# Kernel optimization log

Hardware: AMD Instinct MI355X
Metric: run time of the kernel (lower is better)

## Reference

```python
import jax, jax.numpy as jnp
import numpy as np

SIGMA = 25.0
EPS = 1e-5
TWO_PI = 2.0 * np.pi


def _gn(x, gamma, beta, groups):
    # GroupNorm over (C//G, H, W) per group, per-channel affine.
    B, C, H, W = x.shape
    xg = x.reshape(B, groups, -1)
    m = xg.mean(-1, keepdims=True)
    v = xg.var(-1, keepdims=True)
    xn = ((xg - m) * jax.lax.rsqrt(v + EPS)).reshape(B, C, H, W)
    return xn * gamma[None, :, None, None] + beta[None, :, None, None]


def _conv3(x, k, b):
    y = jax.lax.conv_general_dilated(x, k, (1, 1), 'SAME',
                                     dimension_numbers=('NCHW', 'OIHW', 'NCHW'))
    return y + b[None, :, None, None]


def _tconv2(x, k, b):
    # ConvTranspose2d kernel=2 stride=2 (no overlap) == einsum + reshape.
    # k: [C_in, C_out, 2, 2]
    B, C, H, W = x.shape
    O = k.shape[1]
    y = jnp.einsum('bchw,codq->bohdwq', x, k).reshape(B, O, 2 * H, 2 * W)
    return y + b[None, :, None, None]


def _conv1(x, k, b):
    # 1x1 conv; k: [C_out, C_in]
    return jnp.einsum('bchw,oc->bohw', x, k) + b[None, :, None, None]


def _pool(x):
    B, C, H, W = x.shape
    return x.reshape(B, C, H // 2, 2, W // 2, 2).max(axis=(3, 5))


def _std(t):
    return jnp.sqrt((SIGMA ** (2.0 * t) - 1.0) / (2.0 * jnp.log(SIGMA)))


def setup_inputs() -> dict:
    key = jax.random.key(0)
    ks = jax.random.split(key, 16)
    B, H, W = 64, 128, 128
    E = 2 * W  # 256 = embed_dim

    def w(k, shape, fan_in):
        return jax.random.normal(k, shape, jnp.float32) / np.sqrt(fan_in)

    inp = {
        'x': jax.random.normal(ks[0], (B, 1, H, W), jnp.float32),
        't': jax.random.uniform(ks[1], (B,), jnp.float32, 1e-3, 1.0),
        'Wf': jax.random.normal(ks[2], (H, W), jnp.float32) * 30.0,  # fixed Fourier features
        'fc1_w': w(ks[3], (E, E), E),
        'fc1_b': jnp.zeros((E,), jnp.float32),
        'conv1_k': w(ks[4], (6, 1, 3, 3), 9),
        'conv1_b': jnp.zeros((6,), jnp.float32),
        'gn1_g': jnp.ones((6,), jnp.float32), 'gn1_b': jnp.zeros((6,), jnp.float32),
        'conv2_k': w(ks[5], (24, 6, 3, 3), 6 * 9),
        'conv2_b': jnp.zeros((24,), jnp.float32),
        'gn2_g': jnp.ones((24,), jnp.float32), 'gn2_b': jnp.zeros((24,), jnp.float32),
        't3_k': w(ks[6], (24, 24, 2, 2), 24 * 4),
        't3_b': jnp.zeros((24,), jnp.float32),
        'gn3_g': jnp.ones((48,), jnp.float32), 'gn3_b': jnp.zeros((48,), jnp.float32),
        't4_k': w(ks[7], (48, 12, 2, 2), 48 * 4),
        't4_b': jnp.zeros((12,), jnp.float32),
        'gn4_g': jnp.ones((18,), jnp.float32), 'gn4_b': jnp.zeros((18,), jnp.float32),
        't5_k': w(ks[8], (6, 18), 18),
        't5_b': jnp.zeros((6,), jnp.float32),
        'gn5_g': jnp.ones((6,), jnp.float32), 'gn5_b': jnp.zeros((6,), jnp.float32),
        'fin_k': w(ks[9], (1, 6), 6),
        'fin_b': jnp.zeros((1,), jnp.float32),
    }
    return inp


def reference(x, t, Wf, fc1_w, fc1_b, conv1_k, conv1_b, gn1_g, gn1_b,
              conv2_k, conv2_b, gn2_g, gn2_b, t3_k, t3_b, gn3_g, gn3_b,
              t4_k, t4_b, gn4_g, gn4_b, t5_k, t5_b, gn5_g, gn5_b,
              fin_k, fin_b):
    # Vectorized Gaussian Fourier projection: [B,1,H,W] -> [B,1,H,2W]
    p = x * Wf[None, None] * TWO_PI
    xe = jnp.concatenate([jnp.sin(p), jnp.cos(p)], axis=-1)
    # fc1 on last dim (embed_dim = 2W)
    xf = jnp.einsum('bchw,ow->bcho', xe, fc1_w) + fc1_b
    c1 = _conv3(xf, conv1_k, conv1_b)                              # [B,6,H,2W]
    p1 = _pool(jax.nn.relu(_gn(c1, gn1_g, gn1_b, 6)))              # [B,6,H/2,W]
    c2 = _conv3(p1, conv2_k, conv2_b)                              # [B,24,H/2,W]
    p2 = _pool(jax.nn.relu(_gn(c2, gn2_g, gn2_b, 24)))             # [B,24,H/4,W/2]
    a = p2 * jax.nn.sigmoid(p2)                                    # SiLU bottleneck
    u3 = _tconv2(a, t3_k, t3_b)                                    # [B,24,H/2,W]
    g3 = _gn(jnp.concatenate([c2, u3], axis=1), gn3_g, gn3_b, 6)   # 48 ch
    u4 = _tconv2(g3, t4_k, t4_b)                                   # [B,12,H,2W]
    g4 = _gn(jnp.concatenate([c1, u4], axis=1), gn4_g, gn4_b, 6)   # 18 ch
    u5 = _conv1(g4, t5_k, t5_b)                                    # [B,6,H,2W]
    g5 = _gn(u5, gn5_g, gn5_b, 6)
    return _conv1(g5, fin_k, fin_b) / _std(t)[:, None, None, None]
```

## Files before the change

kernel.cpp:

```cpp
#include <hip/hip_runtime.h>
#include <hip/hip_bf16.h>
#include <math.h>

#define BB 64
#define HH 128
#define WW 128
#define EE 256
#define HP (HH*EE)
#define H2 64
#define W2 128
#define PL2 (H2*W2)
#define H4 32
#define W4 64
#define PL4 (H4*W4)

typedef __hip_bfloat16 bf;
typedef unsigned short ushortt;
typedef __attribute__((ext_vector_type(8))) __bf16 b8v;
typedef __attribute__((ext_vector_type(4))) float f4v;

__device__ __forceinline__ float tof(bf v)    { return __bfloat162float(v); }
__device__ __forceinline__ bf    tob(float v) { return __float2bfloat16(v); }
__device__ __forceinline__ unsigned int bfbits(float v) {
    return (unsigned int)__builtin_bit_cast(ushortt, __float2bfloat16(v));
}
__device__ __forceinline__ float b2f(unsigned int u16) {
    unsigned int x = u16 << 16;
    return __builtin_bit_cast(float, x);
}
__device__ __forceinline__ void wred2(float& s, float& q) {
    #pragma unroll
    for (int m = 32; m; m >>= 1) {
        s += __shfl_xor(s, m);
        q += __shfl_xor(q, m);
    }
}

__global__ __launch_bounds__(256) void k_fourier_fc1(
    const float* __restrict__ x, const float* __restrict__ Wf,
    const float* __restrict__ fc1_w, const float* __restrict__ fc1_b,
    bf* __restrict__ xf, float* __restrict__ mb)
{
    __shared__ ushortt sA[64*264];
    __shared__ ushortt sB[64*264];
    int t = threadIdx.x;
    for (int i = blockIdx.x*256 + t; i < 9216; i += 512*256) mb[i] = 0.f;
    int rb = blockIdx.x >> 2, cb = blockIdx.x & 3;
    int row0 = rb*64, col0 = cb*64;
    const float TP = 6.2831853071795864769f;
    for (int it = 0; it < 32; ++it) {
        int i = it*256 + t;
        int r = i >> 7, w = i & 127;
        int rg = row0 + r;
        float p = x[(size_t)rg*WW + w] * Wf[(size_t)(rg & (HH-1))*WW + w] * TP;
        sA[r*264 + w]       = (ushortt)bfbits(__sinf(p));
        sA[r*264 + 128 + w] = (ushortt)bfbits(__cosf(p));
    }
    #pragma unroll
    for (int it = 0; it < 16; ++it) {
        int i = it*256 + t;
        int o = i >> 6, c4 = i & 63;
        float4 w4 = *(const float4*)(fc1_w + (size_t)(col0 + o)*EE + c4*4);
        uint2 pk;
        pk.x = bfbits(w4.x) | (bfbits(w4.y) << 16);
        pk.y = bfbits(w4.z) | (bfbits(w4.w) << 16);
        *(uint2*)&sB[o*264 + c4*4] = pk;
    }
    __syncthreads();
    int lane = t & 63, wid = t >> 6;
    int m = lane & 15, kq = (lane >> 4) * 8;
    f4v acc[4] = {};
    const ushortt* aBase = &sA[(wid*16 + m)*264 + kq];
    #pragma unroll
    for (int k0 = 0; k0 < 8; ++k0) {
        b8v av = *(const b8v*)(aBase + k0*32);
        #pragma unroll
        for (int t4 = 0; t4 < 4; ++t4) {
            b8v bv = *(const b8v*)&sB[(t4*16 + m)*264 + k0*32 + kq];
            acc[t4] = __builtin_amdgcn_mfma_f32_16x16x32_bf16(av, bv, acc[t4], 0, 0, 0);
        }
    }
    int rbase = row0 + wid*16 + (lane >> 4)*4;
    #pragma unroll
    for (int t4 = 0; t4 < 4; ++t4) {
        int col = col0 + t4*16 + m;
        float bias = fc1_b[col];
        #pragma unroll
        for (int r = 0; r < 4; ++r)
            xf[(size_t)(rbase + r)*EE + col] = tob(acc[t4][r] + bias);
    }
}

__global__ __launch_bounds__(256) void k_conv1(
    const bf* __restrict__ xf, const float* __restrict__ k,
    const float* __restrict__ bias, bf* __restrict__ c1, float* __restrict__ mc1)
{
    __shared__ ushortt sT[6*272];
    __shared__ float red[4][6][2];
    int t = threadIdx.x;
    int ht = blockIdx.x & 31, b = blockIdx.x >> 5;
    int h0 = ht*4;
    const bf* src = xf + (size_t)b*HP;
    if (t < 192) {
        int r = t >> 5, i = t & 31;
        int gy = h0 - 1 + r;
        uint4 v = {0,0,0,0};
        if (gy >= 0 && gy < HH) v = *(const uint4*)(src + (size_t)gy*EE + i*8);
        *(uint4*)&sT[r*272 + 8 + i*8] = v;
    } else if (t < 204) {
        int e = t - 192;
        int r = e >> 1, s = e & 1;
        uint4 z = {0,0,0,0};
        *(uint4*)&sT[r*272 + s*264] = z;
    }
    __syncthreads();
    int wq = (t & 63)*4, hl = t >> 6;
    int lane = t & 63, wid = t >> 6;
    float v[3][6];
    #pragma unroll
    for (int ky = 0; ky < 3; ++ky)
      #pragma unroll
      for (int j = 0; j < 6; ++j)
        v[ky][j] = b2f((unsigned)sT[(hl+ky)*272 + 7 + wq + j]);
    int h = h0 + hl;
    #pragma unroll
    for (int o = 0; o < 6; ++o) {
        float bv = bias[o];
        float a0=bv, a1=bv, a2=bv, a3=bv;
        #pragma unroll
        for (int ky = 0; ky < 3; ++ky)
          #pragma unroll
          for (int kx = 0; kx < 3; ++kx) {
            float wv = k[o*9 + ky*3 + kx];
            a0 += v[ky][kx+0]*wv;
            a1 += v[ky][kx+1]*wv;
            a2 += v[ky][kx+2]*wv;
            a3 += v[ky][kx+3]*wv;
          }
        uint2 pk;
        pk.x = bfbits(a0) | (bfbits(a1) << 16);
        pk.y = bfbits(a2) | (bfbits(a3) << 16);
        *(uint2*)(c1 + ((size_t)(b*6+o)*HH + h)*EE + wq) = pk;
        float s = a0+a1+a2+a3, q = a0*a0+a1*a1+a2*a2+a3*a3;
        wred2(s, q);
        if (lane == 0) { red[wid][o][0] = s; red[wid][o][1] = q; }
    }
    __syncthreads();
    if (t < 6) {
        float S = 0.f, Q = 0.f;
        #pragma unroll
        for (int wv = 0; wv < 4; ++wv) { S += red[wv][t][0]; Q += red[wv][t][1]; }
        atomicAdd(&mc1[((size_t)b*6 + t)*2],     S);
        atomicAdd(&mc1[((size_t)b*6 + t)*2 + 1], Q);
    }
}

__global__ __launch_bounds__(256) void k_conv2(
    const bf* __restrict__ c1, const float* __restrict__ mc1,
    const float* __restrict__ g1, const float* __restrict__ be1,
    const float* __restrict__ kw, const float* __restrict__ bias,
    bf* __restrict__ c2, float* __restrict__ mc2)
{
    __shared__ ushortt sA[256*64];
    __shared__ ushortt sW[32*64];
    __shared__ ushortt sP[6*4*136];
    __shared__ float ssl[12];
    __shared__ float redS[24], redQ[24];
    int t = threadIdx.x;
    int ht = blockIdx.x & 31, b = blockIdx.x >> 5;
    int h0 = ht*2;
    int lane = t & 63, wid = t >> 6;
    int m = lane & 15, q4 = lane >> 4;
    if (t < 24) { redS[t] = 0.f; redQ[t] = 0.f; }
    if (t < 6) {
        float s = mc1[((size_t)b*6 + t)*2], q = mc1[((size_t)b*6 + t)*2 + 1];
        float mean = s * (1.f/HP);
        float var  = q * (1.f/HP) - mean*mean;
        float rstd = rsqrtf(var + 1e-5f);
        float sc = g1[t]*rstd;
        ssl[t*2] = sc; ssl[t*2+1] = be1[t] - mean*sc;
    }
    for (int i = t; i < 1024; i += 256) ((unsigned*)sW)[i] = 0;
    __syncthreads();
    for (int i = t; i < 3120; i += 256) {
        int c = i / 520, rem = i % 520;
        int ry = rem / 130, rx = rem % 130;
        int gy = h0 - 1 + ry, gx = rx - 1;
        float v = 0.f;
        if (gy >= 0 && gy < H2 && gx >= 0 && gx < W2) {
            const bf* pp = c1 + ((size_t)(b*6+c)*HH + 2*gy)*EE + 2*gx;
            unsigned r0 = *(const unsigned*)pp;
            unsigned r1 = *(const unsigned*)(pp + EE);
            float sc = ssl[c*2], sh = ssl[c*2+1];
            float e0 = fmaxf(b2f(r0 & 0xffff)*sc+sh, 0.f);
            float e1 = fmaxf(b2f(r0 >> 16)   *sc+sh, 0.f);
            float e2 = fmaxf(b2f(r1 & 0xffff)*sc+sh, 0.f);
            float e3 = fmaxf(b2f(r1 >> 16)   *sc+sh, 0.f);
            v = fmaxf(fmaxf(e0,e1), fmaxf(e2,e3));
        }
        sP[c*544 + ry*136 + rx] = (ushortt)bfbits(v);
    }
    for (int e = t; e < 1296; e += 256) {
        int o = e / 54, kk = e % 54;
        sW[o*64 + ((((kk >> 3) ^ (o & 7)) << 3) | (kk & 7))] = (ushortt)bfbits(kw[e]);
    }
    __syncthreads();
    {
        int r = t >> 7, xx = t & 127;
        unsigned u[32];
        #pragma unroll
        for (int p = 0; p < 27; ++p) {
            int k0 = 2*p, k1 = 2*p + 1;
            int c0 = k0/9, y0 = (k0%9)/3, x0 = k0%3;
            int c1i = k1/9, y1 = (k1%9)/3, x1 = k1%3;
            unsigned lo = sP[c0*544 + (r+y0)*136 + xx + x0];
            unsigned hi = sP[c1i*544 + (r+y1)*136 + xx + x1];
            u[p] = lo | (hi << 16);
        }
        #pragma unroll
        for (int p = 27; p < 32; ++p) u[p] = 0;
        #pragma unroll
        for (int e = 0; e < 8; ++e) {
            uint4 pk; pk.x = u[4*e]; pk.y = u[4*e+1]; pk.z = u[4*e+2]; pk.w = u[4*e+3];
            *(uint4*)&sA[t*64 + ((e ^ (t & 7)) << 3)] = pk;
        }
    }
    __syncthreads();
    b8v wv[2][2];
    #pragma unroll
    for (int nt = 0; nt < 2; ++nt) {
        int o = nt*16 + m;
        #pragma unroll
        for (int ks = 0; ks < 2; ++ks)
            wv[nt][ks] = *(const b8v*)&sW[o*64 + (((ks*4 + q4) ^ (o & 7)) << 3)];
    }
    f4v acc[4][2] = {};
    #pragma unroll
    for (int mt = 0; mt < 4; ++mt) {
        int px = wid*64 + mt*16 + m;
        b8v a0 = *(const b8v*)&sA[px*64 + (((q4)     ^ (px & 7)) << 3)];
        b8v a1 = *(const b8v*)&sA[px*64 + (((4 + q4) ^ (px & 7)) << 3)];
        #pragma unroll
        for (int nt = 0; nt < 2; ++nt) {
            acc[mt][nt] = __builtin_amdgcn_mfma_f32_16x16x32_bf16(a0, wv[nt][0], acc[mt][nt], 0, 0, 0);
            acc[mt][nt] = __builtin_amdgcn_mfma_f32_16x16x32_bf16(a1, wv[nt][1], acc[mt][nt], 0, 0, 0);
        }
    }
    float sAcc[2] = {0.f, 0.f}, qAcc[2] = {0.f, 0.f};
    #pragma unroll
    for (int nt = 0; nt < 2; ++nt) {
        int o = nt*16 + m;
        bool valid = (o < 24);
        float bo = valid ? bias[o] : 0.f;
        #pragma unroll
        for (int mt = 0; mt < 4; ++mt) {
            int pxb = wid*64 + mt*16 + q4*4;
            unsigned l0 = bfbits(acc[mt][nt][0] + bo);
            unsigned l1 = bfbits(acc[mt][nt][1] + bo);
            unsigned l2 = bfbits(acc[mt][nt][2] + bo);
            unsigned l3 = bfbits(acc[mt][nt][3] + bo);
            if (valid) {
                uint2 pk; pk.x = l0 | (l1 << 16); pk.y = l2 | (l3 << 16);
                int r = pxb >> 7, xx = pxb & 127;
                *(uint2*)(c2 + ((size_t)(b*24+o))*PL2 + (size_t)(h0 + r)*W2 + xx) = pk;
                float f0 = b2f(l0), f1 = b2f(l1), f2 = b2f(l2), f3 = b2f(l3);
                sAcc[nt] += f0+f1+f2+f3;
                qAcc[nt] += f0*f0+f1*f1+f2*f2+f3*f3;
            }
        }
    }
    #pragma unroll
    for (int nt = 0; nt < 2; ++nt) {
        int o = nt*16 + m;
        float s = sAcc[nt], q = qAcc[nt];
        s += __shfl_xor(s, 16); q += __shfl_xor(q, 16);
        s += __shfl_xor(s, 32); q += __shfl_xor(q, 32);
        if (q4 == 0 && o < 24) { atomicAdd(&redS[o], s); atomicAdd(&redQ[o], q); }
    }
    __syncthreads();
    if (t < 24) {
        atomicAdd(&mc2[((size_t)b*24 + t)*2],     redS[t]);
        atomicAdd(&mc2[((size_t)b*24 + t)*2 + 1], redQ[t]);
    }
}

__global__ __launch_bounds__(256) void k_tconv3(
    const bf* __restrict__ c2, const float* __restrict__ mc2,
    const float* __restrict__ g2, const float* __restrict__ be2,
    const float* __restrict__ k3, const float* __restrict__ b3,
    bf* __restrict__ u3, float* __restrict__ mu3)
{
    __shared__ ushortt sA[256*64];
    __shared__ ushortt sW[96*64];
    __shared__ float redS[24], redQ[24];
    __shared__ float ssl[48];
    int t = threadIdx.x;
    int b = blockIdx.x >> 3, pg = blockIdx.x & 7;
    int lane = t & 63, wid = t >> 6;
    int m = lane & 15, q4 = lane >> 4;
    if (t < 24) {
        redS[t] = 0.f; redQ[t] = 0.f;
        float s = mc2[((size_t)b*24 + t)*2], q = mc2[((size_t)b*24 + t)*2 + 1];
        float mean = s * (1.f/PL2);
        float var  = q * (1.f/PL2) - mean*mean;
        float rstd = rsqrtf(var + 1e-5f);
        float sc = g2[t]*rstd;
        ssl[t*2] = sc; ssl[t*2+1] = be2[t] - mean*sc;
    }
    if (t < 96) {
        uint4 z = {0,0,0,0};
        *(uint4*)&sW[t*64 + (((3 ^ (t & 3)) + (t & 4)) << 3)] = z;
    }
    #pragma unroll
    for (int j = 0; j < 9; ++j) {
        int e = j*256 + t;
        int c = e / 96, n = e % 96;
        sW[n*64 + (((((c >> 3) ^ (n & 3)) + (n & 4)) << 3) | (c & 7))] =
            (ushortt)bfbits(k3[e]);
    }
    {
        int pix = pg*256 + t;
        int h4 = pix >> 6, w4 = pix & 63;
        const bf* base = c2 + (size_t)b*24*PL2 + (size_t)(2*h4)*W2 + 2*w4;
        #pragma unroll
        for (int g = 0; g < 3; ++g) {
            unsigned pr[4];
            #pragma unroll
            for (int hc = 0; hc < 4; ++hc) {
                unsigned two[2];
                #pragma unroll
                for (int cc = 0; cc < 2; ++cc) {
                    int c = g*8 + hc*2 + cc;
                    const bf* pp = base + (size_t)c*PL2;
                    unsigned r0 = *(const unsigned*)pp;
                    unsigned r1 = *(const unsigned*)(pp + W2);
                    float sc = ssl[c*2], sh = ssl[c*2+1];
                    float e0 = fmaxf(b2f(r0 & 0xffff)*sc+sh, 0.f);
                    float e1 = fmaxf(b2f(r0 >> 16)   *sc+sh, 0.f);
                    float e2 = fmaxf(b2f(r1 & 0xffff)*sc+sh, 0.f);
                    float e3 = fmaxf(b2f(r1 >> 16)   *sc+sh, 0.f);
                    float mm = fmaxf(fmaxf(e0,e1), fmaxf(e2,e3));
                    mm = mm / (1.f + expf(-mm));
                    two[cc] = bfbits(mm);
                }
                pr[hc] = two[0] | (two[1] << 16);
            }
            uint4 pk; pk.x = pr[0]; pk.y = pr[1]; pk.z = pr[2]; pk.w = pr[3];
            *(uint4*)&sA[t*64 + (((g ^ (t & 3)) + (t & 4)) << 3)] = pk;
        }
        uint4 z = {0,0,0,0};
        *(uint4*)&sA[t*64 + (((3 ^ (t & 3)) + (t & 4)) << 3)] = z;
    }
    __syncthreads();
    b8v wv[6];
    #pragma unroll
    for (int nt = 0; nt < 6; ++nt) {
        int n = nt*16 + m;
        wv[nt] = *(const b8v*)&sW[n*64 + (((q4 ^ (n & 3)) + (n & 4)) << 3)];
    }
    f4v acc[4][6] = {};
    #pragma unroll
    for (int mt = 0; mt < 4; ++mt) {
        int px = wid*64 + mt*16 + m;
        b8v av = *(const b8v*)&sA[px*64 + (((q4 ^ (px & 3)) + (px & 4)) << 3)];
        #pragma unroll
        for (int nt = 0; nt < 6; ++nt)
            acc[mt][nt] = __builtin_amdgcn_mfma_f32_16x16x32_bf16(av, wv[nt], acc[mt][nt], 0, 0, 0);
    }
    float sAcc[6] = {}, qAcc[6] = {};
    int qq = m & 1;
    #pragma unroll
    for (int nt = 0; nt < 6; ++nt) {
        int n = nt*16 + m;
        int o = n >> 2, d = (n >> 1) & 1;
        float bo = b3[o];
        #pragma unroll
        for (int mt = 0; mt < 4; ++mt) {
            int pxb = wid*64 + mt*16 + q4*4;
            unsigned wds[4];
            float s = 0.f, q = 0.f;
            #pragma unroll
            for (int r = 0; r < 4; ++r) {
                float v = acc[mt][nt][r] + bo;
                float vp = __shfl_xor(v, 1);
                unsigned lo = bfbits(v), hi = bfbits(vp);
                wds[r] = lo | (hi << 16);
                float f0 = b2f(lo), f1 = b2f(hi);
                s += f0 + f1;
                q += f0*f0 + f1*f1;
            }
            if (qq == 0) {
                int h4 = (pg*256 + pxb) >> 6;
                int w4 = pxb & 63;
                uint4 pk; pk.x = wds[0]; pk.y = wds[1]; pk.z = wds[2]; pk.w = wds[3];
                *(uint4*)(u3 + ((size_t)(b*24 + o))*PL2 + (size_t)(2*h4 + d)*W2 + 2*w4) = pk;
                sAcc[nt] += s; qAcc[nt] += q;
            }
        }
    }
    #pragma unroll
    for (int nt = 0; nt < 6; ++nt) {
        float s = sAcc[nt], q = qAcc[nt];
        s += __shfl_xor(s, 2);  q += __shfl_xor(q, 2);
        s += __shfl_xor(s, 16); q += __shfl_xor(q, 16);
        s += __shfl_xor(s, 32); q += __shfl_xor(q, 32);
        if ((lane & 51) == 0) {
            int o = nt*4 + (m >> 2);
            atomicAdd(&redS[o], s);
            atomicAdd(&redQ[o], q);
        }
    }
    __syncthreads();
    if (t < 24) {
        atomicAdd(&mu3[((size_t)b*24 + t)*2],     redS[t]);
        atomicAdd(&mu3[((size_t)b*24 + t)*2 + 1], redQ[t]);
    }
}

__global__ __launch_bounds__(256) void k_tconv4(
    const bf* __restrict__ c2, const bf* __restrict__ u3,
    const float* __restrict__ mc2, const float* __restrict__ mu3,
    const float* __restrict__ g3, const float* __restrict__ be3,
    const float* __restrict__ k4, const float* __restrict__ bias4,
    bf* __restrict__ u4, float* __restrict__ mu4)
{
    __shared__ ushortt sA[256*64];
    __shared__ ushortt sW[48*64];
    __shared__ float redS[12], redQ[12];
    __shared__ float ssl[96];
    int t = threadIdx.x;
    int b = blockIdx.x >> 5, pg = blockIdx.x & 31;
    int lane = t & 63, wid = t >> 6;
    int m = lane & 15, q4 = lane >> 4;
    if (t < 12) { redS[t] = 0.f; redQ[t] = 0.f; }
    if (t < 6) {
        float s = 0.f, q = 0.f;
        #pragma unroll
        for (int cl = 0; cl < 8; ++cl) {
            int gc = t*8 + cl;
            const float* p = (gc < 24) ? mc2 + ((size_t)b*24 + gc)*2
                                       : mu3 + ((size_t)b*24 + gc - 24)*2;
            s += p[0]; q += p[1];
        }
        float inv_n = 1.f/((float)PL2*8.f);
        float mean = s*inv_n;
        float var  = q*inv_n - mean*mean;
        float rstd = rsqrtf(var + 1e-5f);
        #pragma unroll
        for (int cl = 0; cl < 8; ++cl) {
            int gc = t*8 + cl;
            float sc = g3[gc]*rstd;
            ssl[gc*2] = sc; ssl[gc*2+1] = be3[gc] - mean*sc;
        }
    }
    #pragma unroll
    for (int j = 0; j < 9; ++j) {
        int e = j*256 + t;
        int c = e / 48, n = e % 48;
        sW[n*64 + ((((c >> 3) ^ (n & 7)) << 3) | (c & 7))] = (ushortt)bfbits(k4[e]);
    }
    if (t < 96) {
        uint4 z = {0,0,0,0};
        int n = t >> 1, kb = 6 + (t & 1);
        *(uint4*)&sW[n*64 + ((kb ^ (n & 7)) << 3)] = z;
    }
    {
        int px = t;
        int pix = pg*256 + px;
        const bf* c2p = c2 + (size_t)b*24*PL2 + pix;
        const bf* u3p = u3 + (size_t)b*24*PL2 + pix;
        #pragma unroll
        for (int g = 0; g < 6; ++g) {
            unsigned pr[4];
            #pragma unroll
            for (int hc = 0; hc < 4; ++hc) {
                int c0 = g*8 + hc*2;
                float r0 = (c0 < 24) ? tof(c2p[(size_t)c0*PL2]) : tof(u3p[(size_t)(c0-24)*PL2]);
                float r1 = (c0+1 < 24) ? tof(c2p[(size_t)(c0+1)*PL2]) : tof(u3p[(size_t)(c0+1-24)*PL2]);
                float v0 = r0 * ssl[2*c0]   + ssl[2*c0+1];
                float v1 = r1 * ssl[2*c0+2] + ssl[2*c0+3];
                pr[hc] = bfbits(v0) | (bfbits(v1) << 16);
            }
            uint4 pk; pk.x = pr[0]; pk.y = pr[1]; pk.z = pr[2]; pk.w = pr[3];
            *(uint4*)&sA[px*64 + ((g ^ (px & 7)) << 3)] = pk;
        }
        uint4 z = {0,0,0,0};
        *(uint4*)&sA[px*64 + ((6 ^ (px & 7)) << 3)] = z;
        *(uint4*)&sA[px*64 + ((7 ^ (px & 7)) << 3)] = z;
    }
    __syncthreads();
    b8v bfr[3][2];
    #pragma unroll
    for (int nt = 0; nt < 3; ++nt) {
        int n = nt*16 + m;
        #pragma unroll
        for (int ks = 0; ks < 2; ++ks)
            bfr[nt][ks] = *(const b8v*)&sW[n*64 + (((ks*4 + q4) ^ (n & 7)) << 3)];
    }
    f4v acc[4][3] = {};
    #pragma unroll
    for (int mt = 0; mt < 4; ++mt) {
        int px = wid*64 + mt*16 + m;
        b8v a0 = *(const b8v*)&sA[px*64 + (((q4)     ^ (px & 7)) << 3)];
        b8v a1 = *(const b8v*)&sA[px*64 + (((4 + q4) ^ (px & 7)) << 3)];
        #pragma unroll
        for (int nt = 0; nt < 3; ++nt) {
            acc[mt][nt] = __builtin_amdgcn_mfma_f32_16x16x32_bf16(a0, bfr[nt][0], acc[mt][nt], 0, 0, 0);
            acc[mt][nt] = __builtin_amdgcn_mfma_f32_16x16x32_bf16(a1, bfr[nt][1], acc[mt][nt], 0, 0, 0);
        }
    }
    float sAcc[3] = {0.f, 0.f, 0.f}, qAcc[3] = {0.f, 0.f, 0.f};
    int qq = m & 1;
    #pragma unroll
    for (int nt = 0; nt < 3; ++nt) {
        int n = nt*16 + m;
        int o = n >> 2, d = (n >> 1) & 1;
        float bo = bias4[o];
        #pragma unroll
        for (int mt = 0; mt < 4; ++mt) {
            int pxb = wid*64 + mt*16 + q4*4;
            unsigned wds[4];
            float s = 0.f, q = 0.f;
            #pragma unroll
            for (int r = 0; r < 4; ++r) {
                float v = acc[mt][nt][r] + bo;
                float vp = __shfl_xor(v, 1);
                unsigned lo = bfbits(v), hi = bfbits(vp);
                wds[r] = lo | (hi << 16);
                float f0 = b2f(lo), f1 = b2f(hi);
                s += f0 + f1;
                q += f0*f0 + f1*f1;
            }
            if (qq == 0) {
                int h2 = (pg*256 + pxb) >> 7;
                int w0 = pxb & 127;
                uint4 pk; pk.x = wds[0]; pk.y = wds[1]; pk.z = wds[2]; pk.w = wds[3];
                *(uint4*)(u4 + (((size_t)(b*12 + o))*HH + 2*h2 + d)*EE + 2*w0) = pk;
                sAcc[nt] += s; qAcc[nt] += q;
            }
        }
    }
    #pragma unroll
    for (int nt = 0; nt < 3; ++nt) {
        float s = sAcc[nt], q = qAcc[nt];
        s += __shfl_xor(s, 2);  q += __shfl_xor(q, 2);
        s += __shfl_xor(s, 16); q += __shfl_xor(q, 16);
        s += __shfl_xor(s, 32); q += __shfl_xor(q, 32);
        if ((lane & 51) == 0) {
            int o = nt*4 + (m >> 2);
            atomicAdd(&redS[o], s);
            atomicAdd(&redQ[o], q);
        }
    }
    __syncthreads();
    if (t < 12) {
        atomicAdd(&mu4[((size_t)b*12 + t)*2],     redS[t]);
        atomicAdd(&mu4[((size_t)b*12 + t)*2 + 1], redQ[t]);
    }
}

__global__ __launch_bounds__(256) void k_conv1x1_u5(
    const bf* __restrict__ c1, const bf* __restrict__ u4,
    const float* __restrict__ mc1, const float* __restrict__ mu4,
    const float* __restrict__ g4, const float* __restrict__ be4,
    const float* __restrict__ k, const float* __restrict__ bias,
    bf* __restrict__ u5, float* __restrict__ mu5)
{
    __shared__ float red[4][6][2];
    __shared__ float ssl[36];
    int t = threadIdx.x;
    int b  = blockIdx.x >> 4;
    int pg = blockIdx.x & 15;
    int pix = pg*2048 + t*8;
    int lane = t & 63, wid = t >> 6;
    if (t < 6) {
        float s = 0.f, q = 0.f;
        #pragma unroll
        for (int cl = 0; cl < 3; ++cl) {
            int gc = t*3 + cl;
            const float* p = (gc < 6) ? mc1 + ((size_t)b*6 + gc)*2
                                      : mu4 + ((size_t)b*12 + gc - 6)*2;
            s += p[0]; q += p[1];
        }
        float inv_n = 1.f/((float)HP*3.f);
        float mean = s*inv_n;
        float var  = q*inv_n - mean*mean;
        float rstd = rsqrtf(var + 1e-5f);
        #pragma unroll
        for (int cl = 0; cl < 3; ++cl) {
            int gc = t*3 + cl;
            float sc = g4[gc]*rstd;
            ssl[gc*2] = sc; ssl[gc*2+1] = be4[gc] - mean*sc;
        }
    }
    __syncthreads();
    const bf* c1p = c1 + ((size_t)b*6)*HP + pix;
    const bf* u4p = u4 + ((size_t)b*12)*HP + pix;
    float acc[6][8];
    #pragma unroll
    for (int o = 0; o < 6; ++o) {
        float bv = bias[o];
        #pragma unroll
        for (int j = 0; j < 8; ++j) acc[o][j] = bv;
    }
    #pragma unroll
    for (int c = 0; c < 18; ++c) {
        uint4 r = (c < 6) ? *(const uint4*)(c1p + (size_t)c*HP)
                          : *(const uint4*)(u4p + (size_t)(c-6)*HP);
        float sc = ssl[2*c], sh = ssl[2*c+1];
        float v[8];
        v[0] = b2f(r.x & 0xffff)*sc + sh;  v[1] = b2f(r.x >> 16)*sc + sh;
        v[2] = b2f(r.y & 0xffff)*sc + sh;  v[3] = b2f(r.y >> 16)*sc + sh;
        v[4] = b2f(r.z & 0xffff)*sc + sh;  v[5] = b2f(r.z >> 16)*sc + sh;
        v[6] = b2f(r.w & 0xffff)*sc + sh;  v[7] = b2f(r.w >> 16)*sc + sh;
        #pragma unroll
        for (int o = 0; o < 6; ++o) {
            float wv = k[o*18 + c];
            #pragma unroll
            for (int j = 0; j < 8; ++j) acc[o][j] += v[j]*wv;
        }
    }
    #pragma unroll
    for (int o = 0; o < 6; ++o) {
        uint4 pk;
        pk.x = bfbits(acc[o][0]) | (bfbits(acc[o][1]) << 16);
        pk.y = bfbits(acc[o][2]) | (bfbits(acc[o][3]) << 16);
        pk.z = bfbits(acc[o][4]) | (bfbits(acc[o][5]) << 16);
        pk.w = bfbits(acc[o][6]) | (bfbits(acc[o][7]) << 16);
        *(uint4*)(u5 + ((size_t)(b*6+o))*HP + pix) = pk;
        float s = 0.f, q = 0.f;
        #pragma unroll
        for (int j = 0; j < 8; ++j) { s += acc[o][j]; q += acc[o][j]*acc[o][j]; }
        wred2(s, q);
        if (lane == 0) { red[wid][o][0] = s; red[wid][o][1] = q; }
    }
    __syncthreads();
    if (t < 6) {
        float S = 0.f, Q = 0.f;
        #pragma unroll
        for (int wv = 0; wv < 4; ++wv) { S += red[wv][t][0]; Q += red[wv][t][1]; }
        atomicAdd(&mu5[((size_t)b*6 + t)*2],     S);
        atomicAdd(&mu5[((size_t)b*6 + t)*2 + 1], Q);
    }
}

__global__ __launch_bounds__(256) void k_final(
    const bf* __restrict__ u5, const float* __restrict__ mu5,
    const float* __restrict__ g5, const float* __restrict__ be5,
    const float* __restrict__ k, const float* __restrict__ bias,
    const float* __restrict__ t, float* __restrict__ out)
{
    __shared__ float ssl[12];
    int tt = threadIdx.x;
    int b = blockIdx.x >> 4;
    int pix = ((blockIdx.x & 15)*256 + tt)*8;
    if (tt < 6) {
        float s = mu5[((size_t)b*6 + tt)*2], q = mu5[((size_t)b*6 + tt)*2 + 1];
        float mean = s * (1.f/HP);
        float var  = q * (1.f/HP) - mean*mean;
        float rstd = rsqrtf(var + 1e-5f);
        float sc = g5[tt]*rstd;
        ssl[tt*2] = sc; ssl[tt*2+1] = be5[tt] - mean*sc;
    }
    __syncthreads();
    const bf* up = u5 + (size_t)b*6*HP + pix;
    float bv = bias[0];
    float a[8];
    #pragma unroll
    for (int j = 0; j < 8; ++j) a[j] = bv;
    #pragma unroll
    for (int c = 0; c < 6; ++c) {
        uint4 r = *(const uint4*)(up + (size_t)c*HP);
        float sc = ssl[2*c], sh = ssl[2*c+1];
        float wv = k[c];
        a[0] += (b2f(r.x & 0xffff)*sc + sh) * wv;
        a[1] += (b2f(r.x >> 16)   *sc + sh) * wv;
        a[2] += (b2f(r.y & 0xffff)*sc + sh) * wv;
        a[3] += (b2f(r.y >> 16)   *sc + sh) * wv;
        a[4] += (b2f(r.z & 0xffff)*sc + sh) * wv;
        a[5] += (b2f(r.z >> 16)   *sc + sh) * wv;
        a[6] += (b2f(r.w & 0xffff)*sc + sh) * wv;
        a[7] += (b2f(r.w >> 16)   *sc + sh) * wv;
    }
    float tb = t[b];
    const float lns = 3.2188758248682007492f;
    float var = (expf(2.f*tb*lns) - 1.f) / (2.f*lns);
    float rs = rsqrtf(var);
    float4 o0; o0.x = a[0]*rs; o0.y = a[1]*rs; o0.z = a[2]*rs; o0.w = a[3]*rs;
    float4 o1; o1.x = a[4]*rs; o1.y = a[5]*rs; o1.z = a[6]*rs; o1.w = a[7]*rs;
    float* op = out + (size_t)b*HP + pix;
    *(float4*)op       = o0;
    *(float4*)(op + 4) = o1;
}

extern "C" void kernel_launch(void* const* d_in, const int* in_sizes, int n_in,
                              void* d_out, int out_size, void* d_ws, size_t ws_size,
                              hipStream_t stream)
{
    const float* x       = (const float*)d_in[0];
    const float* t       = (const float*)d_in[1];
    const float* Wf      = (const float*)d_in[2];
    const float* fc1_w   = (const float*)d_in[3];
    const float* fc1_b   = (const float*)d_in[4];
    const float* conv1_k = (const float*)d_in[5];
    const float* conv1_b = (const float*)d_in[6];
    const float* gn1_g   = (const float*)d_in[7];
    const float* gn1_b   = (const float*)d_in[8];
    const float* conv2_k = (const float*)d_in[9];
    const float* conv2_b = (const float*)d_in[10];
    const float* gn2_g   = (const float*)d_in[11];
    const float* gn2_b   = (const float*)d_in[12];
    const float* t3_k    = (const float*)d_in[13];
    const float* t3_b    = (const float*)d_in[14];
    const float* gn3_g   = (const float*)d_in[15];
    const float* gn3_b   = (const float*)d_in[16];
    const float* t4_k    = (const float*)d_in[17];
    const float* t4_b    = (const float*)d_in[18];
    const float* gn4_g   = (const float*)d_in[19];
    const float* gn4_b   = (const float*)d_in[20];
    const float* t5_k    = (const float*)d_in[21];
    const float* t5_b    = (const float*)d_in[22];
    const float* gn5_g   = (const float*)d_in[23];
    const float* gn5_b   = (const float*)d_in[24];
    const float* fin_k   = (const float*)d_in[25];
    const float* fin_b   = (const float*)d_in[26];

    bf* wsb = (bf*)d_ws;
    bf* c1 = wsb;
    bf* c2 = wsb + 12582912;
    bf* u3 = wsb + 25165824;
    bf* u4 = wsb + 37748736;
    bf* xf = wsb + 39845888;
    bf* u5 = wsb + 12582912;
    float* mb = (float*)(wsb + 62914560);
    float* mc1 = mb;
    float* mc2 = mb + 768;
    float* mu3 = mb + 3840;
    float* mu4 = mb + 6912;
    float* mu5 = mb + 8448;

    k_fourier_fc1<<<512, 256, 0, stream>>>(x, Wf, fc1_w, fc1_b, xf, mb);
    k_conv1<<<2048, 256, 0, stream>>>(xf, conv1_k, conv1_b, c1, mc1);
    k_conv2<<<2048, 256, 0, stream>>>(c1, mc1, gn1_g, gn1_b,
                                      conv2_k, conv2_b, c2, mc2);
    k_tconv3<<<512, 256, 0, stream>>>(c2, mc2, gn2_g, gn2_b,
                                      t3_k, t3_b, u3, mu3);
    k_tconv4<<<2048, 256, 0, stream>>>(c2, u3, mc2, mu3, gn3_g, gn3_b,
                                       t4_k, t4_b, u4, mu4);
    k_conv1x1_u5<<<1024, 256, 0, stream>>>(c1, u4, mc1, mu4, gn4_g, gn4_b,
                                           t5_k, t5_b, u5, mu5);
    k_final<<<1024, 256, 0, stream>>>(u5, mu5, gn5_g, gn5_b,
                                      fin_k, fin_b, t, (float*)d_out);
}
```

Measured before the change: 234.0 us.

## Swizzle block order, halve tconv3 tile, simplify staging index math

Remaps block indices in conv1/conv2 so consecutive blocks spread across batches (XCD-aware ordering). Halves the k_tconv3 pixel tile to 128 and doubles its grid for more parallelism, splitting staging work across thread halves. Replaces div/mod indexing in several weight and input staging loops with shift/mask loops, with separate zeroing of halo columns. Uses the fast __expf intrinsic for SiLU and extends the stats zero-fill range.

```diff
diff --git a/kernel.cpp b/kernel.cpp
--- a/kernel.cpp
+++ b/kernel.cpp
@@ -44,7 +44,7 @@
     __shared__ ushortt sA[64*264];
     __shared__ ushortt sB[64*264];
     int t = threadIdx.x;
-    for (int i = blockIdx.x*256 + t; i < 9216; i += 512*256) mb[i] = 0.f;
+    for (int i = blockIdx.x*256 + t; i < 9280; i += 512*256) mb[i] = 0.f;
     int rb = blockIdx.x >> 2, cb = blockIdx.x & 3;
     int row0 = rb*64, col0 = cb*64;
     const float TP = 6.2831853071795864769f;
@@ -98,7 +98,8 @@
     __shared__ ushortt sT[6*272];
     __shared__ float red[4][6][2];
     int t = threadIdx.x;
-    int ht = blockIdx.x & 31, b = blockIdx.x >> 5;
+    int bid = ((blockIdx.x & 7) << 8) | (blockIdx.x >> 3);
+    int ht = bid & 31, b = bid >> 5;
     int h0 = ht*4;
     const bf* src = xf + (size_t)b*HP;
     if (t < 192) {
@@ -167,7 +168,8 @@
     __shared__ float ssl[12];
     __shared__ float redS[24], redQ[24];
     int t = threadIdx.x;
-    int ht = blockIdx.x & 31, b = blockIdx.x >> 5;
+    int bid = ((blockIdx.x & 7) << 8) | (blockIdx.x >> 3);
+    int ht = bid & 31, b = bid >> 5;
     int h0 = ht*2;
     int lane = t & 63, wid = t >> 6;
     int m = lane & 15, q4 = lane >> 4;
@@ -181,13 +183,19 @@
         ssl[t*2] = sc; ssl[t*2+1] = be1[t] - mean*sc;
     }
     for (int i = t; i < 1024; i += 256) ((unsigned*)sW)[i] = 0;
-    __syncthreads();
-    for (int i = t; i < 3120; i += 256) {
-        int c = i / 520, rem = i % 520;
-        int ry = rem / 130, rx = rem % 130;
-        int gy = h0 - 1 + ry, gx = rx - 1;
+    if (t < 48) {
+        int c = t >> 3, e = t & 7;
+        int ry = e >> 1, rx = (e & 1) ? 129 : 0;
+        sP[c*544 + ry*136 + rx] = 0;
+    }
+    __syncthreads();
+    #pragma unroll
+    for (int j = 0; j < 12; ++j) {
+        int i = j*256 + t;
+        int c = i >> 9, ry = (i >> 7) & 3, gx = i & 127;
+        int gy = h0 - 1 + ry;
         float v = 0.f;
-        if (gy >= 0 && gy < H2 && gx >= 0 && gx < W2) {
+        if (gy >= 0 && gy < H2) {
             const bf* pp = c1 + ((size_t)(b*6+c)*HH + 2*gy)*EE + 2*gx;
             unsigned r0 = *(const unsigned*)pp;
             unsigned r1 = *(const unsigned*)(pp + EE);
@@ -198,11 +206,15 @@
             float e3 = fmaxf(b2f(r1 >> 16)   *sc+sh, 0.f);
             v = fmaxf(fmaxf(e0,e1), fmaxf(e2,e3));
         }
-        sP[c*544 + ry*136 + rx] = (ushortt)bfbits(v);
-    }
-    for (int e = t; e < 1296; e += 256) {
-        int o = e / 54, kk = e % 54;
-        sW[o*64 + ((((kk >> 3) ^ (o & 7)) << 3) | (kk & 7))] = (ushortt)bfbits(kw[e]);
+        sP[c*544 + ry*136 + gx + 1] = (ushortt)bfbits(v);
+    }
+    #pragma unroll
+    for (int j = 0; j < 6; ++j) {
+        int i = j*256 + t;
+        int o = i >> 6, kk = i & 63;
+        if (kk < 54)
+            sW[o*64 + ((((kk >> 3) ^ (o & 7)) << 3) | (kk & 7))] =
+                (ushortt)bfbits(kw[o*54 + kk]);
     }
     __syncthreads();
     {
@@ -290,12 +302,12 @@
     const float* __restrict__ k3, const float* __restrict__ b3,
     bf* __restrict__ u3, float* __restrict__ mu3)
 {
-    __shared__ ushortt sA[256*64];
+    __shared__ ushortt sA[128*64];
     __shared__ ushortt sW[96*64];
     __shared__ float redS[24], redQ[24];
     __shared__ float ssl[48];
     int t = threadIdx.x;
-    int b = blockIdx.x >> 3, pg = blockIdx.x & 7;
+    int b = blockIdx.x >> 4, pg = blockIdx.x & 15;
     int lane = t & 63, wid = t >> 6;
     int m = lane & 15, q4 = lane >> 4;
     if (t < 24) {
@@ -312,18 +324,19 @@
         *(uint4*)&sW[t*64 + (((3 ^ (t & 3)) + (t & 4)) << 3)] = z;
     }
     #pragma unroll
-    for (int j = 0; j < 9; ++j) {
-        int e = j*256 + t;
-        int c = e / 96, n = e % 96;
-        sW[n*64 + (((((c >> 3) ^ (n & 3)) + (n & 4)) << 3) | (c & 7))] =
-            (ushortt)bfbits(k3[e]);
+    for (int j = 0; j < 12; ++j) {
+        int i = j*256 + t;
+        int c = i >> 7, n = i & 127;
+        if (n < 96)
+            sW[n*64 + (((((c >> 3) ^ (n & 3)) + (n & 4)) << 3) | (c & 7))] =
+                (ushortt)bfbits(k3[c*96 + n]);
     }
     {
-        int pix = pg*256 + t;
+        int px = t & 127, half = t >> 7;
+        int pix = pg*128 + px;
         int h4 = pix >> 6, w4 = pix & 63;
         const bf* base = c2 + (size_t)b*24*PL2 + (size_t)(2*h4)*W2 + 2*w4;
-        #pragma unroll
-        for (int g = 0; g < 3; ++g) {
+        auto stageG = [&](int g) {
             unsigned pr[4];
             #pragma unroll
             for (int hc = 0; hc < 4; ++hc) {
@@ -340,16 +353,22 @@
                     float e2 = fmaxf(b2f(r1 & 0xffff)*sc+sh, 0.f);
                     float e3 = fmaxf(b2f(r1 >> 16)   *sc+sh, 0.f);
                     float mm = fmaxf(fmaxf(e0,e1), fmaxf(e2,e3));
-                    mm = mm / (1.f + expf(-mm));
+                    mm = mm / (1.f + __expf(-mm));
                     two[cc] = bfbits(mm);
                 }
                 pr[hc] = two[0] | (two[1] << 16);
             }
             uint4 pk; pk.x = pr[0]; pk.y = pr[1]; pk.z = pr[2]; pk.w = pr[3];
-            *(uint4*)&sA[t*64 + (((g ^ (t & 3)) + (t & 4)) << 3)] = pk;
-        }
-        uint4 z = {0,0,0,0};
-        *(uint4*)&sA[t*64 + (((3 ^ (t & 3)) + (t & 4)) << 3)] = z;
+            *(uint4*)&sA[px*64 + (((g ^ (px & 3)) + (px & 4)) << 3)] = pk;
+        };
+        if (half == 0) {
+            stageG(0);
+            stageG(1);
+        } else {
+            stageG(2);
+            uint4 z = {0,0,0,0};
+            *(uint4*)&sA[px*64 + (((3 ^ (px & 3)) + (px & 4)) << 3)] = z;
+        }
     }
     __syncthreads();
     b8v wv[6];
@@ -358,10 +377,10 @@
         int n = nt*16 + m;
         wv[nt] = *(const b8v*)&sW[n*64 + (((q4 ^ (n & 3)) + (n & 4)) << 3)];
     }
-    f4v acc[4][6] = {};
-    #pragma unroll
-    for (int mt = 0; mt < 4; ++mt) {
-        int px = wid*64 + mt*16 + m;
+    f4v acc[2][6] = {};
+    #pragma unroll
+    for (int mt = 0; mt < 2; ++mt) {
+        int px = wid*32 + mt*16 + m;
         b8v av = *(const b8v*)&sA[px*64 + (((q4 ^ (px & 3)) + (px & 4)) << 3)];
         #pragma unroll
         for (int nt = 0; nt < 6; ++nt)
@@ -375,8 +394,8 @@
         int o = n >> 2, d = (n >> 1) & 1;
         float bo = b3[o];
         #pragma unroll
-        for (int mt = 0; mt < 4; ++mt) {
-            int pxb = wid*64 + mt*16 + q4*4;
+        for (int mt = 0; mt < 2; ++mt) {
+            int pxb = wid*32 + mt*16 + q4*4;
             unsigned wds[4];
             float s = 0.f, q = 0.f;
             #pragma unroll
@@ -390,8 +409,9 @@
                 q += f0*f0 + f1*f1;
             }
             if (qq == 0) {
-                int h4 = (pg*256 + pxb) >> 6;
-                int w4 = pxb & 63;
+                int pix = pg*128 + pxb;
+                int h4 = pix >> 6;
+                int w4 = pix & 63;
                 uint4 pk; pk.x = wds[0]; pk.y = wds[1]; pk.z = wds[2]; pk.w = wds[3];
                 *(uint4*)(u3 + ((size_t)(b*24 + o))*PL2 + (size_t)(2*h4 + d)*W2 + 2*w4) = pk;
                 sAcc[nt] += s; qAcc[nt] += q;
@@ -454,10 +474,12 @@
         }
     }
     #pragma unroll
-    for (int j = 0; j < 9; ++j) {
-        int e = j*256 + t;
-        int c = e / 48, n = e % 48;
-        sW[n*64 + ((((c >> 3) ^ (n & 7)) << 3) | (c & 7))] = (ushortt)bfbits(k4[e]);
+    for (int j = 0; j < 12; ++j) {
+        int i = j*256 + t;
+        int c = i >> 6, n = i & 63;
+        if (n < 48)
+            sW[n*64 + ((((c >> 3) ^ (n & 7)) << 3) | (c & 7))] =
+                (ushortt)bfbits(k4[c*48 + n]);
     }
     if (t < 96) {
         uint4 z = {0,0,0,0};
@@ -743,8 +765,8 @@
     k_conv1<<<2048, 256, 0, stream>>>(xf, conv1_k, conv1_b, c1, mc1);
     k_conv2<<<2048, 256, 0, stream>>>(c1, mc1, gn1_g, gn1_b,
                                       conv2_k, conv2_b, c2, mc2);
-    k_tconv3<<<512, 256, 0, stream>>>(c2, mc2, gn2_g, gn2_b,
-                                      t3_k, t3_b, u3, mu3);
+    k_tconv3<<<1024, 256, 0, stream>>>(c2, mc2, gn2_g, gn2_b,
+                                       t3_k, t3_b, u3, mu3);
     k_tconv4<<<2048, 256, 0, stream>>>(c2, u3, mc2, mu3, gn3_g, gn3_b,
                                        t4_k, t4_b, u4, mu4);
     k_conv1x1_u5<<<1024, 256, 0, stream>>>(c1, u4, mc1, mu4, gn4_g, gn4_b,
```

Measured after the change: 228.7 us. -2.3%, faster.
